# Optimization experiments

Measured on AMD Instinct MI355X. Metric: run time of the kernel, lower is better.

## Reference

```python
import jax, jax.numpy as jnp
import numpy as np

DROPOUT_P = 0.2
DROPOUT_KEY = 42  # fixed key: deterministic dropout for the correctness baseline


def setup_inputs() -> dict:
    key = jax.random.key(0)
    kq, kk = jax.random.split(key)
    B, T, D = 4, 1024, 64
    # uniform[0,1): positive so log() in the original is finite (0 maps to -inf,
    # but exp(log q + log k) still yields q*k == 0, consistent with the math)
    q = jax.random.uniform(kq, (B, T, D), dtype=jnp.float32)
    k = jax.random.uniform(kk, (B, T, D), dtype=jnp.float32)
    return {"q": q, "k": k, "T": T, "block_size": T}


def reference(q, k, T, block_size):
    # exp(log(q)_i + log(k)_j) summed over d == sum_d q_id * k_jd == q @ k^T
    # (mathematically identical for the positive inputs the module requires);
    # expressed as a matmul to avoid the (B,T,T,d) blowup while keeping the same math.
    scale = k.shape[-1] ** (-0.5)
    scores = jnp.einsum('bqd,bkd->bqk', q, k) * scale  # (B,T,T)
    causal = jnp.tril(jnp.ones((block_size, block_size), dtype=bool))[:T, :T]
    scores = jnp.where(causal, scores, -jnp.inf)
    probs = jax.nn.softmax(scores, axis=-1)
    # dropout (training mode in original), deterministic key for reproducibility
    keep = jax.random.bernoulli(jax.random.key(DROPOUT_KEY), 1.0 - DROPOUT_P, probs.shape)
    return jnp.where(keep, probs / (1.0 - DROPOUT_P), 0.0)
```

## Files before the change

kernel.cpp:

```cpp
#include <hip/hip_runtime.h>
#include <stdint.h>

#define TT 1024
#define BB 4

typedef __fp16 fp16x2 __attribute__((ext_vector_type(2)));
typedef __fp16 fp16x8 __attribute__((ext_vector_type(8)));
typedef float  floatx4 __attribute__((ext_vector_type(4)));
union U32H2 { uint32_t u; fp16x2 h; };
union U4H8  { uint4 u; fp16x8 h; };

__device__ __forceinline__ uint32_t rotl32(uint32_t x, int d) {
  return (x << d) | (x >> (32 - d));
}

__device__ __forceinline__ bool keep_at(uint32_t i) {
  uint32_t x0 = 0u, x1 = i;
  const uint32_t ks0 = 0u, ks1 = 42u;
  const uint32_t ks2 = 0x1BD11BDAu ^ ks0 ^ ks1;
  x0 += ks0; x1 += ks1;
#define R4(a,b,c,d)                              \
  x0 += x1; x1 = rotl32(x1,(a)); x1 ^= x0;       \
  x0 += x1; x1 = rotl32(x1,(b)); x1 ^= x0;       \
  x0 += x1; x1 = rotl32(x1,(c)); x1 ^= x0;       \
  x0 += x1; x1 = rotl32(x1,(d)); x1 ^= x0;
  R4(13,15,26,6)   x0 += ks1; x1 += ks2 + 1u;
  R4(17,29,16,24)  x0 += ks2; x1 += ks0 + 2u;
  R4(13,15,26,6)   x0 += ks0; x1 += ks1 + 3u;
  R4(17,29,16,24)  x0 += ks1; x1 += ks2 + 4u;
  R4(13,15,26,6)   x0 += ks2; x1 += ks0 + 5u;
#undef R4
  const uint32_t bits = x0 ^ x1;
  const float u = __uint_as_float((bits >> 9) | 0x3f800000u) - 1.0f;
  return u < 0.8f;
}

__device__ __forceinline__ uint32_t pack2(float x, float y) {
  U32H2 t; t.h = __builtin_amdgcn_cvt_pkrtz(x, y);
  return t.u;
}
__device__ __forceinline__ U4H8 pack8(float4 f0, float4 f1) {
  U4H8 d;
  d.u.x = pack2(f0.x, f0.y); d.u.y = pack2(f0.z, f0.w);
  d.u.z = pack2(f1.x, f1.y); d.u.w = pack2(f1.z, f1.w);
  return d;
}

template <int CTRL>
__device__ __forceinline__ float adddpp(float x) {
  const int s =
      __builtin_amdgcn_update_dpp(0, __float_as_int(x), CTRL, 0xF, 0xF, true);
  return x + __int_as_float(s);
}
__device__ __forceinline__ float radd16(float a) {
  a = adddpp<0xB1>(a);  a = adddpp<0x4E>(a);
  a = adddpp<0x141>(a); a = adddpp<0x140>(a);
  return a;
}

__global__ __launch_bounds__(512)
void attn_kernel(const float* __restrict__ Q, const float* __restrict__ K,
                 float* __restrict__ O) {
  __shared__ float redS[16][8];

  const int tid  = threadIdx.x;
  const int wv   = tid >> 6, ln = tid & 63;
  const int colL = ln & 15;
  const int kgrp = ln >> 4;
  const int g    = blockIdx.x & 63;
  const int b    = blockIdx.x >> 6;

  const float4* Qf = reinterpret_cast<const float4*>(Q) + (size_t)b * TT * 16;
  const float4* Kf = reinterpret_cast<const float4*>(K) + (size_t)b * TT * 16;

  const int arow = g + 64 * (ln & 15);
  const U4H8 qa0 = pack8(Qf[arow * 16 + kgrp * 2],     Qf[arow * 16 + kgrp * 2 + 1]);
  const U4H8 qa1 = pack8(Qf[arow * 16 + 8 + kgrp * 2], Qf[arow * 16 + 8 + kgrp * 2 + 1]);

  int rowD[4]; uint32_t obase[4];
#pragma unroll
  for (int r = 0; r < 4; ++r) {
    rowD[r]  = g + 64 * (kgrp * 4 + r);
    obase[r] = ((uint32_t)b << 20) | ((uint32_t)rowD[r] << 10);
  }

  float p[8][4];
  float sAcc[4] = {0.f, 0.f, 0.f, 0.f};
#pragma unroll
  for (int it = 0; it < 8; ++it) {
    const int jt = it * 8 + wv;
    const int jrow = jt * 16 + colL;
    const U4H8 kb0 = pack8(Kf[jrow * 16 + kgrp * 2],
                           Kf[jrow * 16 + kgrp * 2 + 1]);
    const U4H8 kb1 = pack8(Kf[jrow * 16 + 8 + kgrp * 2],
                           Kf[jrow * 16 + 8 + kgrp * 2 + 1]);
    floatx4 acc = {0.f, 0.f, 0.f, 0.f};
    acc = __builtin_amdgcn_mfma_f32_16x16x32_f16(qa0.h, kb0.h, acc, 0, 0, 0);
    acc = __builtin_amdgcn_mfma_f32_16x16x32_f16(qa1.h, kb1.h, acc, 0, 0, 0);
    const int col = jt * 16 + colL;
#pragma unroll
    for (int r = 0; r < 4; ++r) {
      const float e = (col <= rowD[r]) ? __expf(acc[r] * 0.125f) : 0.f;
      p[it][r] = e;
      sAcc[r] += e;
    }
  }
#pragma unroll
  for (int r = 0; r < 4; ++r) sAcc[r] = radd16(sAcc[r]);
  if (colL == 0) {
#pragma unroll
    for (int r = 0; r < 4; ++r) redS[kgrp * 4 + r][wv] = sAcc[r];
  }
  __syncthreads();
  float rs[4];
#pragma unroll
  for (int r = 0; r < 4; ++r) {
    const int m = kgrp * 4 + r;
    float S = 0.f;
#pragma unroll
    for (int w = 0; w < 8; ++w) S += redS[m][w];
    rs[r] = 1.25f / S;
  }

#pragma unroll
  for (int it = 0; it < 8; ++it) {
    const int jt = it * 8 + wv;
#pragma unroll
    for (int r = 0; r < 4; ++r) {
      const int col = jt * 16 + colL;
      float v = 0.f;
      if (g + 64 * (12 + r) >= jt * 16) {
        const float e = (col <= rowD[r]) ? p[it][r] * rs[r] : 0.f;
        v = keep_at(obase[r] + (uint32_t)col) ? e : 0.f;
      }
      O[obase[r] + (uint32_t)col] = v;
    }
  }
}

extern "C" void kernel_launch(void* const* d_in, const int* in_sizes, int n_in,
                              void* d_out, int out_size, void* d_ws, size_t ws_size,
                              hipStream_t stream) {
  const float* q = (const float*)d_in[0];
  const float* k = (const float*)d_in[1];
  float* out = (float*)d_out;
  attn_kernel<<<dim3(BB * 64), 512, 0, stream>>>(q, k, out);
}
```

Baseline: 24.47 us.

## Split fused attention-dropout kernel into score and row-wise dropout kernels

Splits the single kernel into two passes. The first computes the unnormalized exp scores, stores them as fp16 in workspace and writes the per-row reciprocal sums. A second kernel with one block per row applies normalization and Philox-style dropout with vectorized float4 stores. The aim is to spread the expensive per-element hash over many more blocks and get coalesced output writes. In exchange it adds a 8 MB fp16 round trip through global memory, a second launch, and fp16 rounding of the unnormalized scores.

```diff
diff --git a/kernel.cpp b/kernel.cpp
--- a/kernel.cpp
+++ b/kernel.cpp
@@ -59,8 +59,8 @@
 }
 
 __global__ __launch_bounds__(512)
-void attn_kernel(const float* __restrict__ Q, const float* __restrict__ K,
-                 float* __restrict__ O) {
+void score_kernel(const float* __restrict__ Q, const float* __restrict__ K,
+                  _Float16* __restrict__ E, float* __restrict__ RS) {
   __shared__ float redS[16][8];
 
   const int tid  = threadIdx.x;
@@ -84,7 +84,6 @@
     obase[r] = ((uint32_t)b << 20) | ((uint32_t)rowD[r] << 10);
   }
 
-  float p[8][4];
   float sAcc[4] = {0.f, 0.f, 0.f, 0.f};
 #pragma unroll
   for (int it = 0; it < 8; ++it) {
@@ -101,8 +100,8 @@
 #pragma unroll
     for (int r = 0; r < 4; ++r) {
       const float e = (col <= rowD[r]) ? __expf(acc[r] * 0.125f) : 0.f;
-      p[it][r] = e;
       sAcc[r] += e;
+      E[obase[r] + (uint32_t)col] = (_Float16)e;
     }
   }
 #pragma unroll
@@ -112,30 +111,39 @@
     for (int r = 0; r < 4; ++r) redS[kgrp * 4 + r][wv] = sAcc[r];
   }
   __syncthreads();
-  float rs[4];
-#pragma unroll
-  for (int r = 0; r < 4; ++r) {
-    const int m = kgrp * 4 + r;
-    float S = 0.f;
-#pragma unroll
-    for (int w = 0; w < 8; ++w) S += redS[m][w];
-    rs[r] = 1.25f / S;
-  }
-
-#pragma unroll
-  for (int it = 0; it < 8; ++it) {
-    const int jt = it * 8 + wv;
+  if (wv == 0 && colL == 0) {
 #pragma unroll
     for (int r = 0; r < 4; ++r) {
-      const int col = jt * 16 + colL;
-      float v = 0.f;
-      if (g + 64 * (12 + r) >= jt * 16) {
-        const float e = (col <= rowD[r]) ? p[it][r] * rs[r] : 0.f;
-        v = keep_at(obase[r] + (uint32_t)col) ? e : 0.f;
-      }
-      O[obase[r] + (uint32_t)col] = v;
+      const int m = kgrp * 4 + r;
+      float S = 0.f;
+#pragma unroll
+      for (int w = 0; w < 8; ++w) S += redS[m][w];
+      RS[(b << 10) + g + 64 * m] = 1.25f / S;
     }
   }
+}
+
+__global__ __launch_bounds__(256)
+void drop_kernel(const _Float16* __restrict__ E, const float* __restrict__ RS,
+                 float* __restrict__ O) {
+  const int gb  = blockIdx.x;
+  const int row = gb & 1023;
+  const int tid = threadIdx.x;
+  const uint32_t base = (uint32_t)gb << 10;
+  const float rs = RS[gb];
+  const int col0 = tid * 4;
+
+  float4 v = {0.f, 0.f, 0.f, 0.f};
+  if ((tid & ~63) * 4 <= row) {
+    const fp16x2* E2 = reinterpret_cast<const fp16x2*>(E + base + col0);
+    const fp16x2 e01 = E2[0], e23 = E2[1];
+    const uint32_t i0 = base + (uint32_t)col0;
+    if (col0 + 0 <= row) v.x = keep_at(i0 + 0) ? (float)e01[0] * rs : 0.f;
+    if (col0 + 1 <= row) v.y = keep_at(i0 + 1) ? (float)e01[1] * rs : 0.f;
+    if (col0 + 2 <= row) v.z = keep_at(i0 + 2) ? (float)e23[0] * rs : 0.f;
+    if (col0 + 3 <= row) v.w = keep_at(i0 + 3) ? (float)e23[1] * rs : 0.f;
+  }
+  *reinterpret_cast<float4*>(O + base + col0) = v;
 }
 
 extern "C" void kernel_launch(void* const* d_in, const int* in_sizes, int n_in,
@@ -144,5 +152,8 @@
   const float* q = (const float*)d_in[0];
   const float* k = (const float*)d_in[1];
   float* out = (float*)d_out;
-  attn_kernel<<<dim3(BB * 64), 512, 0, stream>>>(q, k, out);
+  _Float16* E = (_Float16*)d_ws;
+  float* RS = (float*)((char*)d_ws + (size_t)BB * TT * TT * 2);
+  score_kernel<<<dim3(BB * 64), 512, 0, stream>>>(q, k, E, RS);
+  drop_kernel<<<dim3(BB * TT), 256, 0, stream>>>(E, RS, out);
 }
```

New measurement: 25.36 us. +3.6%, slower.

## Precast Q and K to fp16 MFMA fragment layout in a separate pass

Applied to the files above, without the earlier changes.

Adds a small pre-pass kernel that converts Q and K to fp16 and writes them to workspace already arranged in MFMA operand fragment order. The attention kernel then reads one coalesced 16-byte load per operand instead of strided fp32 loads plus in-kernel packing. This removes the redundant conversion of K, which every block previously repeated, and the scattered gathers. The cost is an extra kernel launch and a workspace write and read round trip.

```diff
diff --git a/kernel.cpp b/kernel.cpp
--- a/kernel.cpp
+++ b/kernel.cpp
@@ -39,12 +39,6 @@
   U32H2 t; t.h = __builtin_amdgcn_cvt_pkrtz(x, y);
   return t.u;
 }
-__device__ __forceinline__ U4H8 pack8(float4 f0, float4 f1) {
-  U4H8 d;
-  d.u.x = pack2(f0.x, f0.y); d.u.y = pack2(f0.z, f0.w);
-  d.u.z = pack2(f1.x, f1.y); d.u.w = pack2(f1.z, f1.w);
-  return d;
-}
 
 template <int CTRL>
 __device__ __forceinline__ float adddpp(float x) {
@@ -58,9 +52,26 @@
   return a;
 }
 
+__global__ __launch_bounds__(256)
+void cvt_kernel(const float* __restrict__ Q, const float* __restrict__ K,
+                uint32_t* __restrict__ W) {
+  const int t = blockIdx.x * 256 + threadIdx.x;
+  uint4* W4 = reinterpret_cast<uint4*>(W);
+  const bool isK = t >= 32768;
+  const int t2 = t & 32767;
+  const int ln = t2 & 63, c = (t2 >> 6) & 1, tile = (t2 >> 7) & 63, b = t2 >> 13;
+  const int row = tile * (isK ? 16 : 1) + (isK ? (ln & 15) : 64 * (ln & 15));
+  const float4* src = reinterpret_cast<const float4*>(isK ? K : Q) +
+                      ((size_t)(b << 10) + row) * 16 + c * 8 + (ln >> 4) * 2;
+  const float4 f0 = src[0], f1 = src[1];
+  uint4 d;
+  d.x = pack2(f0.x, f0.y); d.y = pack2(f0.z, f0.w);
+  d.z = pack2(f1.x, f1.y); d.w = pack2(f1.z, f1.w);
+  W4[t] = d;
+}
+
 __global__ __launch_bounds__(512)
-void attn_kernel(const float* __restrict__ Q, const float* __restrict__ K,
-                 float* __restrict__ O) {
+void attn_kernel(const uint32_t* __restrict__ W, float* __restrict__ O) {
   __shared__ float redS[16][8];
 
   const int tid  = threadIdx.x;
@@ -70,12 +81,13 @@
   const int g    = blockIdx.x & 63;
   const int b    = blockIdx.x >> 6;
 
-  const float4* Qf = reinterpret_cast<const float4*>(Q) + (size_t)b * TT * 16;
-  const float4* Kf = reinterpret_cast<const float4*>(K) + (size_t)b * TT * 16;
+  const uint4* W4 = reinterpret_cast<const uint4*>(W);
+  const uint4* Qp = W4 + (size_t)b * 8192;
+  const uint4* Kp = W4 + 32768 + (size_t)b * 8192;
 
-  const int arow = g + 64 * (ln & 15);
-  const U4H8 qa0 = pack8(Qf[arow * 16 + kgrp * 2],     Qf[arow * 16 + kgrp * 2 + 1]);
-  const U4H8 qa1 = pack8(Qf[arow * 16 + 8 + kgrp * 2], Qf[arow * 16 + 8 + kgrp * 2 + 1]);
+  U4H8 qa0, qa1;
+  qa0.u = Qp[(g * 2 + 0) * 64 + ln];
+  qa1.u = Qp[(g * 2 + 1) * 64 + ln];
 
   int rowD[4]; uint32_t obase[4];
 #pragma unroll
@@ -89,11 +101,9 @@
 #pragma unroll
   for (int it = 0; it < 8; ++it) {
     const int jt = it * 8 + wv;
-    const int jrow = jt * 16 + colL;
-    const U4H8 kb0 = pack8(Kf[jrow * 16 + kgrp * 2],
-                           Kf[jrow * 16 + kgrp * 2 + 1]);
-    const U4H8 kb1 = pack8(Kf[jrow * 16 + 8 + kgrp * 2],
-                           Kf[jrow * 16 + 8 + kgrp * 2 + 1]);
+    U4H8 kb0, kb1;
+    kb0.u = Kp[(jt * 2 + 0) * 64 + ln];
+    kb1.u = Kp[(jt * 2 + 1) * 64 + ln];
     floatx4 acc = {0.f, 0.f, 0.f, 0.f};
     acc = __builtin_amdgcn_mfma_f32_16x16x32_f16(qa0.h, kb0.h, acc, 0, 0, 0);
     acc = __builtin_amdgcn_mfma_f32_16x16x32_f16(qa1.h, kb1.h, acc, 0, 0, 0);
@@ -144,5 +154,7 @@
   const float* q = (const float*)d_in[0];
   const float* k = (const float*)d_in[1];
   float* out = (float*)d_out;
-  attn_kernel<<<dim3(BB * 64), 512, 0, stream>>>(q, k, out);
+  uint32_t* w = (uint32_t*)d_ws;
+  cvt_kernel<<<dim3(256), 256, 0, stream>>>(q, k, w);
+  attn_kernel<<<dim3(BB * 64), 512, 0, stream>>>(w, out);
 }
```

After: 23.02 us. 5.9% less time.
